# Performance work log

Hardware: AMD Instinct MI355X
Metric: run time of the kernel (lower is better)

## Reference

```python
import jax, jax.numpy as jnp
import numpy as np

P = 4            # parallel_layers
OUT_PER = 1024   # out_features // parallel_layers
IN_F = 4096
OUT_F = 4096
EPS = 1e-6


def setup_inputs() -> dict:
    key = jax.random.key(0)
    ks = jax.random.split(key, 7)
    x = jax.random.normal(ks[0], (4, 2048, IN_F), dtype=jnp.float32)
    vq_weight = jax.random.normal(ks[1], (16384, P, 32), dtype=jnp.float32)
    w_dec = jax.random.normal(ks[2], (P, 32, 256), dtype=jnp.float32) * 0.05
    b_dec = jax.random.normal(ks[3], (P, 256), dtype=jnp.float32) * 0.01
    d_mean = jax.random.normal(ks[4], (P, 1), dtype=jnp.float32) * 0.01
    d_std = jax.random.uniform(ks[5], (P, 1), dtype=jnp.float32, minval=0.01, maxval=0.05)
    bias = jax.random.normal(ks[6], (OUT_F,), dtype=jnp.float32) * 0.02
    return {"x": x, "vq_weight": vq_weight, "w_dec": w_dec, "b_dec": b_dec,
            "d_mean": d_mean, "d_std": d_std, "bias": bias}


def reference(x, vq_weight, w_dec, b_dec, d_mean, d_std, bias):
    # Decoder (fused per-parallel-layer linear): (N,P,L) x (P,L,C) -> (N,P,C)
    stacked = jnp.einsum('npl,plc->npc', vq_weight, w_dec) + b_dec[None, :, :]
    # recover_weight: permute(1,0,2) -> (P, N, C) -> flatten -> denormalize
    w_flat = jnp.transpose(stacked, (1, 0, 2)).reshape(P, -1)
    w_flat = w_flat * (d_std + EPS) + d_mean
    # reshape to (P, out_per, in_features) -> (out_features, in_features)
    w_recon = w_flat.reshape(P, OUT_PER, IN_F).reshape(OUT_F, IN_F)
    # F.linear(x, w_recon, bias)
    out = jnp.einsum('bsi,oi->bso', x, w_recon) + bias
    return out
```

## Files before the change

kernel.cpp:

```cpp
#include <hip/hip_runtime.h>
#include <stdint.h>

#define M_DIM 8192
#define IN_F  4096
#define OUT_F 4096
#define P_LAY 4


typedef __attribute__((ext_vector_type(8))) short short8;
typedef __attribute__((ext_vector_type(4))) float f32x4;

__device__ inline unsigned short f2bf(float f) {
    unsigned int u = __builtin_bit_cast(unsigned int, f);
    u += 0x7fffu + ((u >> 16) & 1u);
    return (unsigned short)(u >> 16);
}

__global__ __launch_bounds__(256)
void prep_tables(const float* __restrict__ vq, const float* __restrict__ wdec,
                 const float* __restrict__ bdec,
                 unsigned short* __restrict__ vqh,
                 unsigned short* __restrict__ wdech) {
    const int b = blockIdx.x;
    if (b < 2048) {
        const int o4  = (b * 256 + threadIdx.x) * 4;
        const int p   = o4 >> 19;
        const int t   = (o4 >> 9) & 1023;
        const int l   = (o4 >> 4) & 31;
        const int i80 = o4 & 15;
        ushort4 pk;
        pk.x = f2bf(vq[((size_t)(t * 16 + i80 + 0) * 4 + p) * 32 + l]);
        pk.y = f2bf(vq[((size_t)(t * 16 + i80 + 1) * 4 + p) * 32 + l]);
        pk.z = f2bf(vq[((size_t)(t * 16 + i80 + 2) * 4 + p) * 32 + l]);
        pk.w = f2bf(vq[((size_t)(t * 16 + i80 + 3) * 4 + p) * 32 + l]);
        *(ushort4*)(vqh + o4) = pk;
    } else {
        const int g4 = ((b - 2048) * 256 + threadIdx.x) * 4;
        const int n  = g4 >> 8;
        const int c0 = g4 & 255;
        float v[4];
        #pragma unroll
        for (int jj = 0; jj < 4; jj++) {
            if      (n < 128)  v[jj] = wdec[g4 + jj];
            else if (n < 132)  v[jj] = bdec[(n - 128) * 256 + c0 + jj];
            else if (n == 132) v[jj] = 1.0f;
            else               v[jj] = 0.0f;
        }
        ushort4 pk;
        pk.x = f2bf(v[0]); pk.y = f2bf(v[1]); pk.z = f2bf(v[2]); pk.w = f2bf(v[3]);
        *(ushort4*)(wdech + g4) = pk;
    }
}

__global__ __launch_bounds__(256, 2)
void gen_y(const float* __restrict__ x, const unsigned short* __restrict__ wdech,
           const float* __restrict__ dmean, const float* __restrict__ dstd,
           unsigned short* __restrict__ y,
           float* __restrict__ rowterm) {
    __shared__ __attribute__((aligned(16))) unsigned short sW[32768];

    const int tid  = threadIdx.x;
    const int lane = tid & 63;
    const int wave = tid >> 6;
    const int fr   = lane & 15;
    const int kg   = lane >> 4;

    #pragma unroll
    for (int it = 0; it < 16; ++it) {
        const int byte = (it * 256 + tid) * 16;
        const int n    = byte >> 9;
        const int swz  = byte ^ ((n & 7) << 4);
        *(int4*)((char*)sW + swz) = *(const int4*)((const char*)wdech + byte);
    }
    __syncthreads();

    const int sb = blockIdx.x * 16 + wave * 4;
    const float* xbase = x + (size_t)sb * IN_F + fr * 256 + kg * 8;
    const int bswz = (fr & 7) << 4;

    f32x4 acc[4][9] = {};
    #pragma unroll 2
    for (int kc = 0; kc < 8; ++kc) {
        short8 a[4];
        #pragma unroll
        for (int mi = 0; mi < 4; ++mi) {
            const float* xp = xbase + (size_t)mi * IN_F + kc * 32;
            float4 u = *(const float4*)(xp);
            float4 v = *(const float4*)(xp + 4);
            short8 t;
            t[0] = (short)f2bf(u.x); t[1] = (short)f2bf(u.y);
            t[2] = (short)f2bf(u.z); t[3] = (short)f2bf(u.w);
            t[4] = (short)f2bf(v.x); t[5] = (short)f2bf(v.y);
            t[6] = (short)f2bf(v.z); t[7] = (short)f2bf(v.w);
            a[mi] = t;
        }
        short8 b[9];
        #pragma unroll
        for (int nt = 0; nt < 8; ++nt) {
            const int byte = ((nt * 16 + fr) * 512 + kc * 64 + kg * 16) ^ bswz;
            b[nt] = *(const short8*)((const char*)sW + byte);
        }
        b[8] = *(const short8*)(wdech + (size_t)(128 + fr) * 256 + kc * 32 + kg * 8);
        #pragma unroll
        for (int mi = 0; mi < 4; ++mi) {
            #pragma unroll
            for (int nt = 0; nt < 9; ++nt)
                acc[mi][nt] = __builtin_amdgcn_mfma_f32_16x16x32_bf16(
                    a[mi], b[nt], acc[mi][nt], 0, 0, 0);
        }
    }

    #pragma unroll
    for (int mi = 0; mi < 4; ++mi) {
        const int s = sb + mi;
        #pragma unroll
        for (int nt = 0; nt < 8; ++nt) {
            ushort4 pk;
            pk.x = f2bf(acc[mi][nt][0]); pk.y = f2bf(acc[mi][nt][1]);
            pk.z = f2bf(acc[mi][nt][2]); pk.w = f2bf(acc[mi][nt][3]);
            const size_t off = ((size_t)((nt >> 1) * M_DIM + s) * 512)
                             + (nt & 1) * 256 + fr * 16 + kg * 4;
            *(ushort4*)(y + off) = pk;
        }
        float cs = acc[mi][8][0] + acc[mi][8][1] + acc[mi][8][2] + acc[mi][8][3];
        cs += __shfl_xor(cs, 16);
        cs += __shfl_xor(cs, 32);
        const float xsum = __shfl(cs, 4);
        if (lane < 4)
            rowterm[s * 4 + lane] = (dstd[lane] + 1e-6f) * cs + dmean[lane] * xsum;
    }
}

__device__ inline void async16(const void* g, void* l) {
    __builtin_amdgcn_global_load_lds(
        (const __attribute__((address_space(1))) void*)g,
        (__attribute__((address_space(3))) void*)l, 16, 0, 0);
}

__global__ __launch_bounds__(256, 4)
void gemm_y(const unsigned short* __restrict__ Y,
            const unsigned short* __restrict__ V,
            const float* __restrict__ rowterm,
            const float* __restrict__ dstd,
            const float* __restrict__ bias,
            float* __restrict__ C) {
    __shared__ __attribute__((aligned(16))) unsigned short sA[2 * 128 * 32];
    __shared__ __attribute__((aligned(16))) unsigned short sB[2 * 128 * 32];

    const int tid  = threadIdx.x;
    const int lane = tid & 63;
    const int wave = tid >> 6;
    const int wm = (wave >> 1) * 64;
    const int wn = (wave & 1) * 64;

    const int m0 = blockIdx.x * 128;
    const int n0 = blockIdx.y * 128;
    const int p  = n0 >> 10;
    const int t0 = n0 & 1023;

    const char* gAb = (const char*)(Y + (size_t)p * M_DIM * 512);
    const char* gBb = (const char*)(V + (size_t)p * 1024  * 512);

    f32x4 acc[4][4] = {};
    for (int k0 = 0; k0 < 512; k0 += 64) {
        __syncthreads();
        #pragma unroll
        for (int q = 0; q < 4; q++) {
            const int u      = wave * 4 + q;
            const int kc     = u >> 3;
            const int rowblk = (u & 7) * 16;
            const int row    = rowblk + (lane >> 2);
            const int cb     = (lane & 3) * 16;
            const size_t gofs = (size_t)k0 * 2 + kc * 64 + cb;
            char* ldst = (char*)sA + kc * 8192 + rowblk * 64 + lane * 16;
            async16(gAb + (size_t)(m0 + row) * 1024 + gofs, ldst);
            ldst = (char*)sB + kc * 8192 + rowblk * 64 + lane * 16;
            async16(gBb + (size_t)(t0 + row) * 1024 + gofs, ldst);
        }
        __syncthreads();

        #pragma unroll
        for (int kc = 0; kc < 2; kc++) {
            short8 bv[4];
            #pragma unroll
            for (int ni = 0; ni < 4; ni++)
                bv[ni] = *(const short8*)((const char*)sB + kc * 8192
                        + (wn + ni * 16 + (lane & 15)) * 64 + (lane >> 4) * 16);
            #pragma unroll
            for (int mi = 0; mi < 4; mi++) {
                short8 av = *(const short8*)((const char*)sA + kc * 8192
                        + (wm + mi * 16 + (lane & 15)) * 64 + (lane >> 4) * 16);
                #pragma unroll
                for (int ni = 0; ni < 4; ni++)
                    acc[mi][ni] = __builtin_amdgcn_mfma_f32_16x16x32_bf16(
                        av, bv[ni], acc[mi][ni], 0, 0, 0);
            }
        }
    }

    const int fr = lane & 15;
    const int rq = (lane >> 4) * 4;
    const float sp = dstd[p] + 1e-6f;
    #pragma unroll
    for (int mi = 0; mi < 4; mi++) {
        const int mb = m0 + wm + mi * 16 + rq;
        float rt[4];
        #pragma unroll
        for (int r = 0; r < 4; r++) rt[r] = rowterm[(mb + r) * 4 + p];
        #pragma unroll
        for (int ni = 0; ni < 4; ni++) {
            const int o = n0 + wn + ni * 16 + fr;
            const float bn = bias[o];
            float* cp = C + (size_t)mb * OUT_F + o;
            #pragma unroll
            for (int r = 0; r < 4; r++)
                cp[(size_t)r * OUT_F] = acc[mi][ni][r] * sp + rt[r] + bn;
        }
    }
}

extern "C" void kernel_launch(void* const* d_in, const int* in_sizes, int n_in,
                              void* d_out, int out_size, void* d_ws, size_t ws_size,
                              hipStream_t stream) {
    const float* x     = (const float*)d_in[0];
    const float* vq    = (const float*)d_in[1];
    const float* wdec  = (const float*)d_in[2];
    const float* bdec  = (const float*)d_in[3];
    const float* dmean = (const float*)d_in[4];
    const float* dstd  = (const float*)d_in[5];
    const float* bias  = (const float*)d_in[6];
    float* out = (float*)d_out;

    unsigned short* y     = (unsigned short*)d_ws;
    unsigned short* vqh   = y + (size_t)4 * M_DIM * 512;
    unsigned short* wdech = vqh + (size_t)4 * 1024 * 512;
    float* rowterm = (float*)(wdech + 144 * 256);

    prep_tables<<<2084, 256, 0, stream>>>(vq, wdec, bdec, vqh, wdech);
    gen_y<<<M_DIM / 16, 256, 0, stream>>>(x, wdech, dmean, dstd, y, rowterm);
    gemm_y<<<dim3(M_DIM / 128, OUT_F / 128), 256, 0, stream>>>(
        y, vqh, rowterm, dstd, bias, out);
}
```

Baseline: 312.7 us.

## Build decoder table in gen_y shared memory per half, shrink row tile for occupancy

Removes the wdech staging table from prep_tables. gen_y now converts w_dec/b_dec to bf16 directly into shared memory, one 128-column half at a time, which cuts LDS from 64KB to 36KB per block. Rows per wave drop from 4 to 2 so the block count doubles and launch bounds allow 3 blocks per CU for better latency hiding. x loads for each half are issued before the barrier to overlap with table construction. In exchange, every block re-reads and re-converts the fp32 decoder weights, and reuse of each B fragment across rows is halved.

```diff
diff --git a/kernel.cpp b/kernel.cpp
--- a/kernel.cpp
+++ b/kernel.cpp
@@ -17,101 +17,98 @@
 }
 
 __global__ __launch_bounds__(256)
-void prep_tables(const float* __restrict__ vq, const float* __restrict__ wdec,
-                 const float* __restrict__ bdec,
-                 unsigned short* __restrict__ vqh,
-                 unsigned short* __restrict__ wdech) {
-    const int b = blockIdx.x;
-    if (b < 2048) {
-        const int o4  = (b * 256 + threadIdx.x) * 4;
-        const int p   = o4 >> 19;
-        const int t   = (o4 >> 9) & 1023;
-        const int l   = (o4 >> 4) & 31;
-        const int i80 = o4 & 15;
-        ushort4 pk;
-        pk.x = f2bf(vq[((size_t)(t * 16 + i80 + 0) * 4 + p) * 32 + l]);
-        pk.y = f2bf(vq[((size_t)(t * 16 + i80 + 1) * 4 + p) * 32 + l]);
-        pk.z = f2bf(vq[((size_t)(t * 16 + i80 + 2) * 4 + p) * 32 + l]);
-        pk.w = f2bf(vq[((size_t)(t * 16 + i80 + 3) * 4 + p) * 32 + l]);
-        *(ushort4*)(vqh + o4) = pk;
-    } else {
-        const int g4 = ((b - 2048) * 256 + threadIdx.x) * 4;
-        const int n  = g4 >> 8;
-        const int c0 = g4 & 255;
-        float v[4];
-        #pragma unroll
-        for (int jj = 0; jj < 4; jj++) {
-            if      (n < 128)  v[jj] = wdec[g4 + jj];
-            else if (n < 132)  v[jj] = bdec[(n - 128) * 256 + c0 + jj];
-            else if (n == 132) v[jj] = 1.0f;
-            else               v[jj] = 0.0f;
-        }
-        ushort4 pk;
-        pk.x = f2bf(v[0]); pk.y = f2bf(v[1]); pk.z = f2bf(v[2]); pk.w = f2bf(v[3]);
-        *(ushort4*)(wdech + g4) = pk;
-    }
-}
-
-__global__ __launch_bounds__(256, 2)
-void gen_y(const float* __restrict__ x, const unsigned short* __restrict__ wdech,
-           const float* __restrict__ dmean, const float* __restrict__ dstd,
+void prep_tables(const float* __restrict__ vq, unsigned short* __restrict__ vqh) {
+    const int o4  = (blockIdx.x * 256 + threadIdx.x) * 4;
+    const int p   = o4 >> 19;
+    const int t   = (o4 >> 9) & 1023;
+    const int l   = (o4 >> 4) & 31;
+    const int i80 = o4 & 15;
+    ushort4 pk;
+    pk.x = f2bf(vq[((size_t)(t * 16 + i80 + 0) * 4 + p) * 32 + l]);
+    pk.y = f2bf(vq[((size_t)(t * 16 + i80 + 1) * 4 + p) * 32 + l]);
+    pk.z = f2bf(vq[((size_t)(t * 16 + i80 + 2) * 4 + p) * 32 + l]);
+    pk.w = f2bf(vq[((size_t)(t * 16 + i80 + 3) * 4 + p) * 32 + l]);
+    *(ushort4*)(vqh + o4) = pk;
+}
+
+__global__ __launch_bounds__(256, 3)
+void gen_y(const float* __restrict__ x, const float* __restrict__ wdec,
+           const float* __restrict__ bdec, const float* __restrict__ dmean,
+           const float* __restrict__ dstd,
            unsigned short* __restrict__ y,
            float* __restrict__ rowterm) {
-    __shared__ __attribute__((aligned(16))) unsigned short sW[32768];
+    __shared__ __attribute__((aligned(16))) unsigned short sW[18432];
 
     const int tid  = threadIdx.x;
     const int lane = tid & 63;
     const int wave = tid >> 6;
     const int fr   = lane & 15;
     const int kg   = lane >> 4;
+    const int bswz = (fr & 7) << 4;
+    const int sb   = blockIdx.x * 8 + wave * 2;
+
+    f32x4 acc[2][9] = {};
 
     #pragma unroll
-    for (int it = 0; it < 16; ++it) {
-        const int byte = (it * 256 + tid) * 16;
-        const int n    = byte >> 9;
-        const int swz  = byte ^ ((n & 7) << 4);
-        *(int4*)((char*)sW + swz) = *(const int4*)((const char*)wdech + byte);
-    }
-    __syncthreads();
-
-    const int sb = blockIdx.x * 16 + wave * 4;
-    const float* xbase = x + (size_t)sb * IN_F + fr * 256 + kg * 8;
-    const int bswz = (fr & 7) << 4;
-
-    f32x4 acc[4][9] = {};
-    #pragma unroll 2
-    for (int kc = 0; kc < 8; ++kc) {
-        short8 a[4];
-        #pragma unroll
-        for (int mi = 0; mi < 4; ++mi) {
-            const float* xp = xbase + (size_t)mi * IN_F + kc * 32;
-            float4 u = *(const float4*)(xp);
-            float4 v = *(const float4*)(xp + 4);
-            short8 t;
-            t[0] = (short)f2bf(u.x); t[1] = (short)f2bf(u.y);
-            t[2] = (short)f2bf(u.z); t[3] = (short)f2bf(u.w);
-            t[4] = (short)f2bf(v.x); t[5] = (short)f2bf(v.y);
-            t[6] = (short)f2bf(v.z); t[7] = (short)f2bf(v.w);
-            a[mi] = t;
-        }
-        short8 b[9];
-        #pragma unroll
-        for (int nt = 0; nt < 8; ++nt) {
-            const int byte = ((nt * 16 + fr) * 512 + kc * 64 + kg * 16) ^ bswz;
-            b[nt] = *(const short8*)((const char*)sW + byte);
-        }
-        b[8] = *(const short8*)(wdech + (size_t)(128 + fr) * 256 + kc * 32 + kg * 8);
-        #pragma unroll
-        for (int mi = 0; mi < 4; ++mi) {
-            #pragma unroll
-            for (int nt = 0; nt < 9; ++nt)
-                acc[mi][nt] = __builtin_amdgcn_mfma_f32_16x16x32_bf16(
-                    a[mi], b[nt], acc[mi][nt], 0, 0, 0);
+    for (int h = 0; h < 2; ++h) {
+        if (h) __syncthreads();
+        #pragma unroll
+        for (int it = 0; it < 18; ++it) {
+            const int idx = it * 256 + tid;
+            const int n   = idx >> 5;
+            const int c4  = (idx & 31) * 4;
+            const int cg  = h * 128 + c4;
+            float4 v;
+            if (n < 128)       v = *(const float4*)(wdec + n * 256 + cg);
+            else if (n < 132)  v = *(const float4*)(bdec + (n - 128) * 256 + cg);
+            else if (n == 132) v = float4{1.f, 1.f, 1.f, 1.f};
+            else               v = float4{0.f, 0.f, 0.f, 0.f};
+            ushort4 pk;
+            pk.x = f2bf(v.x); pk.y = f2bf(v.y); pk.z = f2bf(v.z); pk.w = f2bf(v.w);
+            *(ushort4*)((char*)sW + n * 256 + ((c4 * 2) ^ ((n & 7) << 4))) = pk;
+        }
+        float4 xu[2][4], xv[2][4];
+        #pragma unroll
+        for (int mi = 0; mi < 2; ++mi) {
+            #pragma unroll
+            for (int kc = 0; kc < 4; ++kc) {
+                const float* xp = x + (size_t)(sb + mi) * IN_F + fr * 256
+                                + h * 128 + kc * 32 + kg * 8;
+                xu[mi][kc] = *(const float4*)(xp);
+                xv[mi][kc] = *(const float4*)(xp + 4);
+            }
+        }
+        __syncthreads();
+        short8 a[2][4];
+        #pragma unroll
+        for (int mi = 0; mi < 2; ++mi) {
+            #pragma unroll
+            for (int kc = 0; kc < 4; ++kc) {
+                short8 t;
+                t[0] = (short)f2bf(xu[mi][kc].x); t[1] = (short)f2bf(xu[mi][kc].y);
+                t[2] = (short)f2bf(xu[mi][kc].z); t[3] = (short)f2bf(xu[mi][kc].w);
+                t[4] = (short)f2bf(xv[mi][kc].x); t[5] = (short)f2bf(xv[mi][kc].y);
+                t[6] = (short)f2bf(xv[mi][kc].z); t[7] = (short)f2bf(xv[mi][kc].w);
+                a[mi][kc] = t;
+            }
+        }
+        #pragma unroll
+        for (int nt = 0; nt < 9; ++nt) {
+            #pragma unroll
+            for (int kc = 0; kc < 4; ++kc) {
+                const short8 b = *(const short8*)((const char*)sW
+                               + (nt * 16 + fr) * 256
+                               + ((kc * 64 + kg * 16) ^ bswz));
+                acc[0][nt] = __builtin_amdgcn_mfma_f32_16x16x32_bf16(
+                    a[0][kc], b, acc[0][nt], 0, 0, 0);
+                acc[1][nt] = __builtin_amdgcn_mfma_f32_16x16x32_bf16(
+                    a[1][kc], b, acc[1][nt], 0, 0, 0);
+            }
         }
     }
 
     #pragma unroll
-    for (int mi = 0; mi < 4; ++mi) {
+    for (int mi = 0; mi < 2; ++mi) {
         const int s = sb + mi;
         #pragma unroll
         for (int nt = 0; nt < 8; ++nt) {
@@ -231,13 +228,12 @@
     const float* bias  = (const float*)d_in[6];
     float* out = (float*)d_out;
 
-    unsigned short* y     = (unsigned short*)d_ws;
-    unsigned short* vqh   = y + (size_t)4 * M_DIM * 512;
-    unsigned short* wdech = vqh + (size_t)4 * 1024 * 512;
-    float* rowterm = (float*)(wdech + 144 * 256);
-
-    prep_tables<<<2084, 256, 0, stream>>>(vq, wdec, bdec, vqh, wdech);
-    gen_y<<<M_DIM / 16, 256, 0, stream>>>(x, wdech, dmean, dstd, y, rowterm);
+    unsigned short* y   = (unsigned short*)d_ws;
+    unsigned short* vqh = y + (size_t)4 * M_DIM * 512;
+    float* rowterm = (float*)(vqh + (size_t)4 * 1024 * 512);
+
+    prep_tables<<<2048, 256, 0, stream>>>(vq, vqh);
+    gen_y<<<M_DIM / 8, 256, 0, stream>>>(x, wdec, bdec, dmean, dstd, y, rowterm);
     gemm_y<<<dim3(M_DIM / 128, OUT_F / 128), 256, 0, stream>>>(
         y, vqh, rowterm, dstd, bias, out);
 }
```

Measured after the change: 332.5 us. 6.4% more time.

## Shrink gen_y per-wave rows, prefetch x, and remap gemm_y blocks for locality

Applied to the files above, without the earlier changes.

gen_y now handles 2 rows per wave instead of 4, doubling the grid, raising launch bounds to 4 blocks per CU, and software-prefetching the next x chunk into registers while the MFMAs run. The B fragment is loaded per-nt inside the loop to cut register pressure. gemm_y switches to a 1D grid with a remapped block order (interleaving by lin&7) meant to improve L2 reuse or spread blocks across XCDs. The smaller gen_y tile means the 64KB shared weight table is loaded twice as often per row of output, and with 64KB of LDS per block the occupancy target of 4 blocks per CU may not actually be reached.

```diff
diff --git a/kernel.cpp b/kernel.cpp
--- a/kernel.cpp
+++ b/kernel.cpp
@@ -52,7 +52,7 @@
     }
 }
 
-__global__ __launch_bounds__(256, 2)
+__global__ __launch_bounds__(256, 4)
 void gen_y(const float* __restrict__ x, const unsigned short* __restrict__ wdech,
            const float* __restrict__ dmean, const float* __restrict__ dstd,
            unsigned short* __restrict__ y,
@@ -64,6 +64,8 @@
     const int wave = tid >> 6;
     const int fr   = lane & 15;
     const int kg   = lane >> 4;
+    const int bswz = (fr & 7) << 4;
+    const int sb   = blockIdx.x * 8 + wave * 2;
 
     #pragma unroll
     for (int it = 0; it < 16; ++it) {
@@ -72,46 +74,51 @@
         const int swz  = byte ^ ((n & 7) << 4);
         *(int4*)((char*)sW + swz) = *(const int4*)((const char*)wdech + byte);
     }
+
+    const float* xb0 = x + (size_t)sb * IN_F + fr * 256 + kg * 8;
+    float4 xu[2], xv[2];
+    #pragma unroll
+    for (int mi = 0; mi < 2; ++mi) {
+        xu[mi] = *(const float4*)(xb0 + (size_t)mi * IN_F);
+        xv[mi] = *(const float4*)(xb0 + (size_t)mi * IN_F + 4);
+    }
     __syncthreads();
 
-    const int sb = blockIdx.x * 16 + wave * 4;
-    const float* xbase = x + (size_t)sb * IN_F + fr * 256 + kg * 8;
-    const int bswz = (fr & 7) << 4;
-
-    f32x4 acc[4][9] = {};
-    #pragma unroll 2
+    f32x4 acc[2][9] = {};
+    #pragma unroll
     for (int kc = 0; kc < 8; ++kc) {
-        short8 a[4];
-        #pragma unroll
-        for (int mi = 0; mi < 4; ++mi) {
-            const float* xp = xbase + (size_t)mi * IN_F + kc * 32;
-            float4 u = *(const float4*)(xp);
-            float4 v = *(const float4*)(xp + 4);
+        short8 a[2];
+        #pragma unroll
+        for (int mi = 0; mi < 2; ++mi) {
             short8 t;
-            t[0] = (short)f2bf(u.x); t[1] = (short)f2bf(u.y);
-            t[2] = (short)f2bf(u.z); t[3] = (short)f2bf(u.w);
-            t[4] = (short)f2bf(v.x); t[5] = (short)f2bf(v.y);
-            t[6] = (short)f2bf(v.z); t[7] = (short)f2bf(v.w);
+            t[0] = (short)f2bf(xu[mi].x); t[1] = (short)f2bf(xu[mi].y);
+            t[2] = (short)f2bf(xu[mi].z); t[3] = (short)f2bf(xu[mi].w);
+            t[4] = (short)f2bf(xv[mi].x); t[5] = (short)f2bf(xv[mi].y);
+            t[6] = (short)f2bf(xv[mi].z); t[7] = (short)f2bf(xv[mi].w);
             a[mi] = t;
         }
-        short8 b[9];
-        #pragma unroll
-        for (int nt = 0; nt < 8; ++nt) {
-            const int byte = ((nt * 16 + fr) * 512 + kc * 64 + kg * 16) ^ bswz;
-            b[nt] = *(const short8*)((const char*)sW + byte);
-        }
-        b[8] = *(const short8*)(wdech + (size_t)(128 + fr) * 256 + kc * 32 + kg * 8);
-        #pragma unroll
-        for (int mi = 0; mi < 4; ++mi) {
-            #pragma unroll
-            for (int nt = 0; nt < 9; ++nt)
-                acc[mi][nt] = __builtin_amdgcn_mfma_f32_16x16x32_bf16(
-                    a[mi], b[nt], acc[mi][nt], 0, 0, 0);
-        }
-    }
-
-    #pragma unroll
-    for (int mi = 0; mi < 4; ++mi) {
+        if (kc < 7) {
+            #pragma unroll
+            for (int mi = 0; mi < 2; ++mi) {
+                xu[mi] = *(const float4*)(xb0 + (size_t)mi * IN_F + (kc + 1) * 32);
+                xv[mi] = *(const float4*)(xb0 + (size_t)mi * IN_F + (kc + 1) * 32 + 4);
+            }
+        }
+        #pragma unroll
+        for (int nt = 0; nt < 9; ++nt) {
+            short8 b;
+            if (nt < 8)
+                b = *(const short8*)((const char*)sW
+                    + (((nt * 16 + fr) * 512 + kc * 64 + kg * 16) ^ bswz));
+            else
+                b = *(const short8*)(wdech + (size_t)(128 + fr) * 256 + kc * 32 + kg * 8);
+            acc[0][nt] = __builtin_amdgcn_mfma_f32_16x16x32_bf16(a[0], b, acc[0][nt], 0, 0, 0);
+            acc[1][nt] = __builtin_amdgcn_mfma_f32_16x16x32_bf16(a[1], b, acc[1][nt], 0, 0, 0);
+        }
+    }
+
+    #pragma unroll
+    for (int mi = 0; mi < 2; ++mi) {
         const int s = sb + mi;
         #pragma unroll
         for (int nt = 0; nt < 8; ++nt) {
@@ -153,10 +160,13 @@
     const int wm = (wave >> 1) * 64;
     const int wn = (wave & 1) * 64;
 
-    const int m0 = blockIdx.x * 128;
-    const int n0 = blockIdx.y * 128;
-    const int p  = n0 >> 10;
-    const int t0 = n0 & 1023;
+    const int lin  = blockIdx.x;
+    const int wg   = (lin & 7) * 256 + (lin >> 3);
+    const int p    = wg >> 9;
+    const int rest = wg & 511;
+    const int m0   = (rest >> 3) * 128;
+    const int t0   = (rest & 7) * 128;
+    const int n0   = p * 1024 + t0;
 
     const char* gAb = (const char*)(Y + (size_t)p * M_DIM * 512);
     const char* gBb = (const char*)(V + (size_t)p * 1024  * 512);
@@ -237,7 +247,6 @@
     float* rowterm = (float*)(wdech + 144 * 256);
 
     prep_tables<<<2084, 256, 0, stream>>>(vq, wdec, bdec, vqh, wdech);
-    gen_y<<<M_DIM / 16, 256, 0, stream>>>(x, wdech, dmean, dstd, y, rowterm);
-    gemm_y<<<dim3(M_DIM / 128, OUT_F / 128), 256, 0, stream>>>(
-        y, vqh, rowterm, dstd, bias, out);
-}
+    gen_y<<<M_DIM / 8, 256, 0, stream>>>(x, wdech, dmean, dstd, y, rowterm);
+    gemm_y<<<2048, 256, 0, stream>>>(y, vqh, rowterm, dstd, bias, out);
+}
```

Result: faster. 284.5 us (-9.0%).
